# Kernel optimization log

Measured on AMD Instinct MI355X. Metric: run time of the kernel, lower is better.

## Reference

```python
import jax, jax.numpy as jnp
import numpy as np

B, IN_DIM, MEM = 8192, 4096, 256
MIN_TS, MAX_TS, EPS = 0.1, 10.0, 1e-6
LN_EPS = 1e-5


def setup_inputs() -> dict:
    key = jax.random.key(0)
    ks = jax.random.split(key, 10)
    std = 0.02
    d_in = MEM + IN_DIM  # 4352
    return {
        "x": jax.random.normal(ks[0], (B, IN_DIM), jnp.float32),
        "h": jax.random.normal(ks[1], (B, MEM), jnp.float32),
        # memory_target: Linear(d_in, 2*MEM) -> LN -> GELU -> Linear(2*MEM, MEM)
        "W1": std * jax.random.normal(ks[2], (d_in, 2 * MEM), jnp.float32),
        "b1": jnp.zeros((2 * MEM,), jnp.float32),
        "g1": jnp.ones((2 * MEM,), jnp.float32),
        "be1": jnp.zeros((2 * MEM,), jnp.float32),
        "W2": std * jax.random.normal(ks[3], (2 * MEM, MEM), jnp.float32),
        "b2": jnp.zeros((MEM,), jnp.float32),
        # decay_gate: Linear(d_in, MEM) -> sigmoid
        "Wd": std * jax.random.normal(ks[4], (d_in, MEM), jnp.float32),
        "bd": jnp.zeros((MEM,), jnp.float32),
        # input_gate: Linear(d_in, MEM) -> sigmoid
        "Wu": std * jax.random.normal(ks[5], (d_in, MEM), jnp.float32),
        "bu": jnp.zeros((MEM,), jnp.float32),
    }


def _layernorm(t, g, b):
    mu = jnp.mean(t, axis=-1, keepdims=True)
    var = jnp.mean(jnp.square(t - mu), axis=-1, keepdims=True)
    return (t - mu) * jax.lax.rsqrt(var + LN_EPS) * g + b


def reference(x, h, W1, b1, g1, be1, W2, b2, Wd, bd, Wu, bu):
    combined = jnp.concatenate([h, x], axis=-1)  # [B, MEM+IN_DIM]
    # memory_target branch: Linear -> LayerNorm -> GELU (exact) -> Linear -> tanh
    t = _layernorm(combined @ W1 + b1, g1, be1)
    t = jax.nn.gelu(t, approximate=False)
    h_candidate = jnp.tanh(t @ W2 + b2)  # [B, MEM]
    # gates
    decay = jax.nn.sigmoid(combined @ Wd + bd)
    update = jax.nn.sigmoid(combined @ Wu + bu)
    decay = MIN_TS + (MAX_TS - MIN_TS) * decay + EPS
    new_h = (1.0 - update) * (h / decay) + update * h_candidate
    # normalize_memory: rescale new_h to old h's L2 norm
    h_norm = jnp.maximum(jnp.linalg.norm(h, axis=-1, keepdims=True), EPS)
    nh_norm = jnp.maximum(jnp.linalg.norm(new_h, axis=-1, keepdims=True), 1e-12)
    new_h = new_h / nh_norm * h_norm
    return new_h
```

## Files before the change

### kernel.cpp

```cpp
#include <hip/hip_runtime.h>
#include <stdint.h>

typedef unsigned short u16;

#define B_ROWS 8192
#define IN_DIM 4096
#define MEM 256
#define D_IN 4352
#define N1 1024
#define K2 512
#define LN_EPS 1e-5f

typedef __attribute__((ext_vector_type(4))) float f32x4;
typedef __attribute__((ext_vector_type(4))) uint32_t u32x4;
typedef __attribute__((ext_vector_type(4))) unsigned short u16x4;
typedef __attribute__((ext_vector_type(8))) short bf16x8;

#define AS1(p) ((__attribute__((address_space(1))) void*)(p))
#define AS3(p) ((__attribute__((address_space(3))) void*)(p))

__device__ __forceinline__ float bf2f(u16 u) {
  union { uint32_t u; float f; } c; c.u = ((uint32_t)u) << 16; return c.f;
}
__device__ __forceinline__ u16 f2bf(float f) {
  union { float f; uint32_t u; } c; c.f = f;
  uint32_t r = (c.u + 0x7fffu + ((c.u >> 16) & 1u)) >> 16;
  return (u16)r;
}
__device__ __forceinline__ uint32_t fbits(float f) {
  union { float f; uint32_t u; } c; c.f = f; return c.u;
}
__device__ __forceinline__ uint32_t pack_rne(float a, float b) {
  return ((uint32_t)f2bf(b) << 16) | f2bf(a);
}
__device__ __forceinline__ uint32_t pack_trunc(float a, float b) {
  return (fbits(b) & 0xFFFF0000u) | (fbits(a) >> 16);
}

__global__ __launch_bounds__(256)
void prep_kernel(const float* __restrict__ W1, const float* __restrict__ Wd,
                 const float* __restrict__ Wu, const float* __restrict__ W2,
                 const float* __restrict__ h, const float* __restrict__ x,
                 u16* __restrict__ WT, u16* __restrict__ W2F, u16* __restrict__ Abf) {
  __shared__ u16 tile[64][68];
  const int blk = blockIdx.x, t = threadIdx.x;
  if (blk < 1088) {
    int n0 = (blk & 15) * 64, k0 = (blk >> 4) * 64;
    const float* src; int srcN, ns0;
    if (n0 < 512)      { src = W1; srcN = 512; ns0 = n0; }
    else if (n0 < 768) { src = Wd; srcN = 256; ns0 = n0 - 512; }
    else               { src = Wu; srcN = 256; ns0 = n0 - 768; }
    int rr = t >> 4;
    int c4 = (t & 15) * 4;
#pragma unroll
    for (int i = 0; i < 4; i++) {
      int k = i * 16 + rr;
      f32x4 v = *(const f32x4*)&src[(size_t)(k0 + k) * srcN + ns0 + c4];
      tile[c4 + 0][k] = f2bf(v[0]);
      tile[c4 + 1][k] = f2bf(v[1]);
      tile[c4 + 2][k] = f2bf(v[2]);
      tile[c4 + 3][k] = f2bf(v[3]);
    }
    __syncthreads();
#pragma unroll
    for (int i = 0; i < 4; i++) {
      int n = i * 16 + rr;
      u16x4 w;
      w.x = tile[n][c4 + 0];
      w.y = tile[n][c4 + 1];
      w.z = tile[n][c4 + 2];
      w.w = tile[n][c4 + 3];
      *(u16x4*)&WT[(size_t)(n0 + n) * D_IN + k0 + c4] = w;
    }
  } else if (blk < 1104) {
    int kw = blk - 1088;
#pragma unroll
    for (int q = 0; q < 4; q++) {
      float v[8];
#pragma unroll
      for (int j = 0; j < 8; j++)
        v[j] = W2[(size_t)(kw * 32 + q * 8 + j) * 256 + t];
      u32x4 w;
      w.x = pack_rne(v[0], v[1]);
      w.y = pack_rne(v[2], v[3]);
      w.z = pack_rne(v[4], v[5]);
      w.w = pack_rne(v[6], v[7]);
      *(u32x4*)&W2F[(size_t)((kw * 4 + q) * 256 + t) * 8] = w;
    }
  } else {
    int b = blk - 1104;
    const float* src; int r, dcol;
    if (b < 1024) {
      int g = (b * 256 + t) * 8;
      src = h + g; r = g >> 8; dcol = g & 255;
    } else {
      int g = ((b - 1024) * 256 + t) * 8;
      src = x + g; r = g >> 12; dcol = MEM + (g & 4095);
    }
    f32x4 v0 = *(const f32x4*)src;
    f32x4 v1 = *(const f32x4*)(src + 4);
    u32x4 w;
    w.x = pack_rne(v0[0], v0[1]);
    w.y = pack_rne(v0[2], v0[3]);
    w.z = pack_rne(v1[0], v1[1]);
    w.w = pack_rne(v1[2], v1[3]);
    *(u32x4*)&Abf[(size_t)r * D_IN + dcol] = w;
  }
}

__global__ __launch_bounds__(256, 4)
void gemm1_pre_kernel(const u16* __restrict__ Abf, const u16* __restrict__ WT,
                      u16* __restrict__ G0, u16* __restrict__ G1, int klen) {
  __shared__ __attribute__((aligned(16))) u16 As[128 * 64];
  __shared__ __attribute__((aligned(16))) u16 Bs[128 * 64];
  const int t = threadIdx.x;
  const int lane = t & 63, wave = t >> 6;
  const int by = blockIdx.x & 63;
  const int bx = (blockIdx.x >> 6) & 7;
  const int part = blockIdx.x >> 9;
  const int kbase = part * klen;
  u16* __restrict__ Gout = part ? G1 : G0;
  const int row0 = by * 128, col0 = bx * 128;
  const int q = lane >> 4, mrow = lane & 15;
  const int wm = wave >> 1, wn = wave & 1;

  int ar[4], ac[4];
#pragma unroll
  for (int j = 0; j < 4; j++) {
    int idx = j * 256 + t;
    int r = idx >> 3;
    ar[j] = r;
    ac[j] = (idx & 7) ^ (r & 7);
  }

  f32x4 acc[4][4] = {};

  for (int k0 = kbase; k0 < kbase + klen; k0 += 64) {
#pragma unroll
    for (int j = 0; j < 4; j++) {
      const u16* gp = WT + (size_t)(col0 + ar[j]) * D_IN + k0 + ac[j] * 8;
      __builtin_amdgcn_global_load_lds(AS1(gp), AS3(&Bs[(j * 256 + t) * 8]), 16, 0, 0);
    }
#pragma unroll
    for (int j = 0; j < 4; j++) {
      const u16* gp = Abf + (size_t)(row0 + ar[j]) * D_IN + k0 + ac[j] * 8;
      __builtin_amdgcn_global_load_lds(AS1(gp), AS3(&As[(j * 256 + t) * 8]), 16, 0, 0);
    }
    __syncthreads();
#pragma unroll
    for (int kk = 0; kk < 2; kk++) {
      bf16x8 a[4], b[4];
#pragma unroll
      for (int mt = 0; mt < 4; mt++) {
        int row = wm * 64 + mt * 16 + mrow;
        int p = (kk * 4 + q) ^ (mrow & 7);
        a[mt] = *(const bf16x8*)&As[row * 64 + p * 8];
      }
#pragma unroll
      for (int nt = 0; nt < 4; nt++) {
        int row = wn * 64 + nt * 16 + mrow;
        int p = (kk * 4 + q) ^ (mrow & 7);
        b[nt] = *(const bf16x8*)&Bs[row * 64 + p * 8];
      }
#pragma unroll
      for (int mt = 0; mt < 4; mt++) {
#pragma unroll
        for (int nt = 0; nt < 4; nt++) {
          acc[mt][nt] = __builtin_amdgcn_mfma_f32_16x16x32_bf16(a[mt], b[nt], acc[mt][nt], 0, 0, 0);
        }
      }
    }
    __syncthreads();
  }
#pragma unroll
  for (int mt = 0; mt < 4; mt++) {
#pragma unroll
    for (int nt = 0; nt < 4; nt++) {
#pragma unroll
      for (int i = 0; i < 4; i++) {
        int row = row0 + wm * 64 + mt * 16 + q * 4 + i;
        int col = col0 + wn * 64 + nt * 16 + mrow;
        Gout[(size_t)row * N1 + col] = f2bf(acc[mt][nt][i]);
      }
    }
  }
}

__global__ __launch_bounds__(256, 4)
void gemm1_inline_kernel(const float* __restrict__ x, const float* __restrict__ h,
                         const u16* __restrict__ WT, u16* __restrict__ G0,
                         u16* __restrict__ G1, int klen) {
  __shared__ __attribute__((aligned(16))) u16 As[128 * 64];
  __shared__ __attribute__((aligned(16))) u16 Bs[128 * 64];
  const int t = threadIdx.x;
  const int lane = t & 63, wave = t >> 6;
  const int by = blockIdx.x & 63;
  const int bx = (blockIdx.x >> 6) & 7;
  const int part = blockIdx.x >> 9;
  const int kbase = part * klen;
  u16* __restrict__ Gout = part ? G1 : G0;
  const int row0 = by * 128, col0 = bx * 128;
  const int q = lane >> 4, mrow = lane & 15;
  const int wm = wave >> 1, wn = wave & 1;

  int ar[4], ac[4];
#pragma unroll
  for (int j = 0; j < 4; j++) {
    int idx = j * 256 + t;
    int r = idx >> 3;
    ar[j] = r;
    ac[j] = (idx & 7) ^ (r & 7);
  }
  f32x4 acc[4][4] = {};
  for (int k0 = kbase; k0 < kbase + klen; k0 += 64) {
#pragma unroll
    for (int j = 0; j < 4; j++) {
      const u16* gp = WT + (size_t)(col0 + ar[j]) * D_IN + k0 + ac[j] * 8;
      __builtin_amdgcn_global_load_lds(AS1(gp), AS3(&Bs[(j * 256 + t) * 8]), 16, 0, 0);
    }
#pragma unroll
    for (int j = 0; j < 4; j++) {
      int k = k0 + ac[j] * 8;
      const float* gp = (k < MEM) ? (h + (size_t)(row0 + ar[j]) * MEM + k)
                                  : (x + (size_t)(row0 + ar[j]) * IN_DIM + (k - MEM));
      f32x4 v0 = *(const f32x4*)gp;
      f32x4 v1 = *(const f32x4*)(gp + 4);
      u32x4 w;
      w.x = pack_trunc(v0[0], v0[1]);
      w.y = pack_trunc(v0[2], v0[3]);
      w.z = pack_trunc(v1[0], v1[1]);
      w.w = pack_trunc(v1[2], v1[3]);
      *(u32x4*)&As[(j * 256 + t) * 8] = w;
    }
    __syncthreads();
#pragma unroll
    for (int kk = 0; kk < 2; kk++) {
      bf16x8 a[4], b[4];
#pragma unroll
      for (int mt = 0; mt < 4; mt++) {
        int row = wm * 64 + mt * 16 + mrow;
        int p = (kk * 4 + q) ^ (mrow & 7);
        a[mt] = *(const bf16x8*)&As[row * 64 + p * 8];
      }
#pragma unroll
      for (int nt = 0; nt < 4; nt++) {
        int row = wn * 64 + nt * 16 + mrow;
        int p = (kk * 4 + q) ^ (mrow & 7);
        b[nt] = *(const bf16x8*)&Bs[row * 64 + p * 8];
      }
#pragma unroll
      for (int mt = 0; mt < 4; mt++) {
#pragma unroll
        for (int nt = 0; nt < 4; nt++) {
          acc[mt][nt] = __builtin_amdgcn_mfma_f32_16x16x32_bf16(a[mt], b[nt], acc[mt][nt], 0, 0, 0);
        }
      }
    }
    __syncthreads();
  }
#pragma unroll
  for (int mt = 0; mt < 4; mt++) {
#pragma unroll
    for (int nt = 0; nt < 4; nt++) {
#pragma unroll
      for (int i = 0; i < 4; i++) {
        int row = row0 + wm * 64 + mt * 16 + q * 4 + i;
        int col = col0 + wn * 64 + nt * 16 + mrow;
        Gout[(size_t)row * N1 + col] = f2bf(acc[mt][nt][i]);
      }
    }
  }
}

__global__ __launch_bounds__(256, 4)
void fused_ln_gemm2_kernel(const u16* __restrict__ G0, const u16* __restrict__ G1,
                           const u16* __restrict__ W2F, const float* __restrict__ h,
                           const float* __restrict__ b1v, const float* __restrict__ g1v,
                           const float* __restrict__ be1v, const float* __restrict__ b2,
                           const float* __restrict__ bd, const float* __restrict__ bu,
                           float* __restrict__ out, int nparts) {
  __shared__ __attribute__((aligned(16))) u16 As[16 * 512];
  __shared__ float redA[16][4], redB[16][4], scl[16];
  const int t = threadIdx.x, lane = t & 63, wave = t >> 6;
  const int q = lane >> 4, mrow = lane & 15;
  const int r0 = blockIdx.x * 16;

  {
    const int lr = t & 15;
    const int lc = t >> 4;
    float z[32];
    const u16* g0p = G0 + (size_t)(r0 + lr) * N1 + lc * 32;
    const u16* g1p = G1 + (size_t)(r0 + lr) * N1 + lc * 32;
    float s = 0.f, ss = 0.f;
#pragma unroll
    for (int j = 0; j < 4; j++) {
      u32x4 w0 = *(const u32x4*)(g0p + j * 8);
      u32x4 w1;
      if (nparts == 2) w1 = *(const u32x4*)(g1p + j * 8);
#pragma unroll
      for (int e = 0; e < 4; e++) {
        float lo = bf2f((u16)(w0[e] & 0xffff));
        float hi = bf2f((u16)(w0[e] >> 16));
        if (nparts == 2) {
          lo += bf2f((u16)(w1[e] & 0xffff));
          hi += bf2f((u16)(w1[e] >> 16));
        }
        int cb = lc * 32 + j * 8 + e * 2;
        lo += b1v[cb];
        hi += b1v[cb + 1];
        z[j * 8 + e * 2] = lo;
        z[j * 8 + e * 2 + 1] = hi;
        s += lo + hi;
        ss += lo * lo + hi * hi;
      }
    }
    s += __shfl_xor(s, 16, 64);  s += __shfl_xor(s, 32, 64);
    ss += __shfl_xor(ss, 16, 64); ss += __shfl_xor(ss, 32, 64);
    if (lane < 16) { redA[lr][wave] = s; redB[lr][wave] = ss; }
    __syncthreads();
    float S  = redA[lr][0] + redA[lr][1] + redA[lr][2] + redA[lr][3];
    float SS = redB[lr][0] + redB[lr][1] + redB[lr][2] + redB[lr][3];
    float mu = S * (1.0f / 512.0f);
    float var = SS * (1.0f / 512.0f) - mu * mu;
    float rstd = rsqrtf(var + LN_EPS);
#pragma unroll
    for (int j = 0; j < 4; j++) {
      u32x4 wpk;
#pragma unroll
      for (int e = 0; e < 4; e++) {
        int cb = lc * 32 + j * 8 + e * 2;
        float y0 = (z[j * 8 + e * 2] - mu) * rstd * g1v[cb] + be1v[cb];
        float y1 = (z[j * 8 + e * 2 + 1] - mu) * rstd * g1v[cb + 1] + be1v[cb + 1];
        float o0 = 0.5f * y0 * (1.0f + erff(y0 * 0.7071067811865475f));
        float o1 = 0.5f * y1 * (1.0f + erff(y1 * 0.7071067811865475f));
        wpk[e] = pack_rne(o0, o1);
      }
      int p = lc * 4 + j;
      int ps = p ^ (lr & 7);
      *(u32x4*)&As[lr * 512 + ps * 8] = wpk;
    }
  }
  __syncthreads();

  f32x4 acc[4] = {};
#pragma unroll
  for (int kw = 0; kw < 16; kw++) {
    int pa = (kw * 4 + q) ^ (mrow & 7);
    bf16x8 a = *(const bf16x8*)&As[mrow * 512 + pa * 8];
#pragma unroll
    for (int nt = 0; nt < 4; nt++) {
      const u16* bp = W2F + (size_t)((kw * 4 + q) * 256 + wave * 64 + nt * 16 + mrow) * 8;
      bf16x8 b = *(const bf16x8*)bp;
      acc[nt] = __builtin_amdgcn_mfma_f32_16x16x32_bf16(a, b, acc[nt], 0, 0, 0);
    }
  }
  __syncthreads();

  float snh[4], shh[4];
#pragma unroll
  for (int i = 0; i < 4; i++) {
    int r = q * 4 + i;
    size_t grow = (size_t)(r0 + r);
    float a_nh = 0.f, a_h = 0.f;
#pragma unroll
    for (int nt = 0; nt < 4; nt++) {
      int c = wave * 64 + nt * 16 + mrow;
      float hc = tanhf(acc[nt][i] + b2[c]);
      float zd = bf2f(G0[grow * N1 + 512 + c]);
      float zu = bf2f(G0[grow * N1 + 768 + c]);
      if (nparts == 2) {
        zd += bf2f(G1[grow * N1 + 512 + c]);
        zu += bf2f(G1[grow * N1 + 768 + c]);
      }
      zd += bd[c];
      zu += bu[c];
      float dec = 0.1f + 9.9f / (1.0f + expf(-zd)) + 1e-6f;
      float u = 1.0f / (1.0f + expf(-zu));
      float hv = h[grow * MEM + c];
      float nh = (1.0f - u) * (hv / dec) + u * hc;
      acc[nt][i] = nh;
      a_nh += nh * nh;
      a_h += hv * hv;
    }
    snh[i] = a_nh;
    shh[i] = a_h;
  }
#pragma unroll
  for (int m = 1; m <= 8; m <<= 1) {
#pragma unroll
    for (int i = 0; i < 4; i++) {
      snh[i] += __shfl_xor(snh[i], m, 64);
      shh[i] += __shfl_xor(shh[i], m, 64);
    }
  }
  if (mrow == 0) {
#pragma unroll
    for (int i = 0; i < 4; i++) {
      int r = q * 4 + i;
      redA[r][wave] = snh[i];
      redB[r][wave] = shh[i];
    }
  }
  __syncthreads();
  if (t < 16) {
    float tn = redA[t][0] + redA[t][1] + redA[t][2] + redA[t][3];
    float th = redB[t][0] + redB[t][1] + redB[t][2] + redB[t][3];
    float hn = fmaxf(sqrtf(th), 1e-6f);
    float nn = fmaxf(sqrtf(tn), 1e-12f);
    scl[t] = hn / nn;
  }
  __syncthreads();
#pragma unroll
  for (int i = 0; i < 4; i++) {
    int r = q * 4 + i;
    size_t grow = (size_t)(r0 + r);
    float sc = scl[r];
#pragma unroll
    for (int nt = 0; nt < 4; nt++) {
      int c = wave * 64 + nt * 16 + mrow;
      out[grow * MEM + c] = acc[nt][i] * sc;
    }
  }
}

extern "C" void kernel_launch(void* const* d_in, const int* in_sizes, int n_in,
                              void* d_out, int out_size, void* d_ws, size_t ws_size,
                              hipStream_t stream) {
  const float* x   = (const float*)d_in[0];
  const float* h   = (const float*)d_in[1];
  const float* W1  = (const float*)d_in[2];
  const float* b1  = (const float*)d_in[3];
  const float* g1  = (const float*)d_in[4];
  const float* be1 = (const float*)d_in[5];
  const float* W2  = (const float*)d_in[6];
  const float* b2  = (const float*)d_in[7];
  const float* Wd  = (const float*)d_in[8];
  const float* bd  = (const float*)d_in[9];
  const float* Wu  = (const float*)d_in[10];
  const float* bu  = (const float*)d_in[11];
  float* out = (float*)d_out;

  char* ws = (char*)d_ws;
  u16* WT  = (u16*)(ws);
  u16* W2F = (u16*)(ws + 8912896);
  u16* G0  = (u16*)(ws + 9175040);
  u16* G1  = (u16*)(ws + 25952256);
  u16* Abf = (u16*)(ws + 42729472);

  const int nparts = (ws_size >= 42729472u) ? 2 : 1;
  const int klen = D_IN / nparts;
  const bool use_pre = (ws_size >= 114032640u);

  if (use_pre) {
    prep_kernel<<<18512, 256, 0, stream>>>(W1, Wd, Wu, W2, h, x, WT, W2F, Abf);
    gemm1_pre_kernel<<<512 * nparts, 256, 0, stream>>>(Abf, WT, G0, G1, klen);
  } else {
    prep_kernel<<<1104, 256, 0, stream>>>(W1, Wd, Wu, W2, h, x, WT, W2F, Abf);
    gemm1_inline_kernel<<<512 * nparts, 256, 0, stream>>>(x, h, WT, G0, G1, klen);
  }

  fused_ln_gemm2_kernel<<<B_ROWS / 16, 256, 0, stream>>>(G0, G1, W2F, h, b1, g1, be1,
                                                         b2, bd, bu, out, nparts);
}
```

Measured before the change: 338.5 us.

## Replace GEMM1 with 256x256-tile double-buffered pipelined kernel with block swizzle

Replaces the 128x128 single-buffered first GEMM with a 512-thread kernel computing 256x256 tiles. It double-buffers LDS, interleaves async global-to-LDS loads with MFMA phases using explicit vmcnt waits and barriers, and raises wave priority during MFMA. A block-index swizzle groups blocks for cache locality. The aim is to hide load latency and raise arithmetic intensity. In exchange it uses 128KB of LDS per block, larger accumulator register use, and launches only 256 blocks, so occupancy and load balance are at risk.

```diff
diff --git a/kernel.cpp b/kernel.cpp
--- a/kernel.cpp
+++ b/kernel.cpp
@@ -108,83 +108,128 @@
   }
 }
 
-__global__ __launch_bounds__(256, 4)
-void gemm1_pre_kernel(const u16* __restrict__ Abf, const u16* __restrict__ WT,
-                      u16* __restrict__ G0, u16* __restrict__ G1, int klen) {
-  __shared__ __attribute__((aligned(16))) u16 As[128 * 64];
-  __shared__ __attribute__((aligned(16))) u16 Bs[128 * 64];
+#define BAR() { asm volatile("" ::: "memory"); __builtin_amdgcn_s_barrier(); asm volatile("" ::: "memory"); }
+#define VMW4() asm volatile("s_waitcnt vmcnt(4)" ::: "memory");
+#define VMW0() asm volatile("s_waitcnt vmcnt(0)" ::: "memory");
+
+__global__ __launch_bounds__(512, 2)
+void gemm1_pre256_kernel(const u16* __restrict__ Abf, const u16* __restrict__ WT,
+                         u16* __restrict__ G0, u16* __restrict__ G1, int klen) {
+  __shared__ __attribute__((aligned(16))) u16 As[2][16384];
+  __shared__ __attribute__((aligned(16))) u16 Bs[2][16384];
   const int t = threadIdx.x;
   const int lane = t & 63, wave = t >> 6;
-  const int by = blockIdx.x & 63;
-  const int bx = (blockIdx.x >> 6) & 7;
-  const int part = blockIdx.x >> 9;
+  const int bid = (int)blockIdx.x;
+  const int swz = (bid & 7) * 32 + (bid >> 3);
+  const int by = swz & 31;
+  const int bx = (swz >> 5) & 3;
+  const int part = swz >> 7;
   const int kbase = part * klen;
   u16* __restrict__ Gout = part ? G1 : G0;
-  const int row0 = by * 128, col0 = bx * 128;
+  const int row0 = by * 256, col0 = bx * 256;
   const int q = lane >> 4, mrow = lane & 15;
-  const int wm = wave >> 1, wn = wave & 1;
-
-  int ar[4], ac[4];
-#pragma unroll
-  for (int j = 0; j < 4; j++) {
-    int idx = j * 256 + t;
-    int r = idx >> 3;
-    ar[j] = r;
-    ac[j] = (idx & 7) ^ (r & 7);
-  }
-
-  f32x4 acc[4][4] = {};
-
-  for (int k0 = kbase; k0 < kbase + klen; k0 += 64) {
-#pragma unroll
-    for (int j = 0; j < 4; j++) {
-      const u16* gp = WT + (size_t)(col0 + ar[j]) * D_IN + k0 + ac[j] * 8;
-      __builtin_amdgcn_global_load_lds(AS1(gp), AS3(&Bs[(j * 256 + t) * 8]), 16, 0, 0);
-    }
-#pragma unroll
-    for (int j = 0; j < 4; j++) {
-      const u16* gp = Abf + (size_t)(row0 + ar[j]) * D_IN + k0 + ac[j] * 8;
-      __builtin_amdgcn_global_load_lds(AS1(gp), AS3(&As[(j * 256 + t) * 8]), 16, 0, 0);
-    }
-    __syncthreads();
-#pragma unroll
-    for (int kk = 0; kk < 2; kk++) {
-      bf16x8 a[4], b[4];
-#pragma unroll
-      for (int mt = 0; mt < 4; mt++) {
-        int row = wm * 64 + mt * 16 + mrow;
-        int p = (kk * 4 + q) ^ (mrow & 7);
-        a[mt] = *(const bf16x8*)&As[row * 64 + p * 8];
-      }
-#pragma unroll
-      for (int nt = 0; nt < 4; nt++) {
-        int row = wn * 64 + nt * 16 + mrow;
-        int p = (kk * 4 + q) ^ (mrow & 7);
-        b[nt] = *(const bf16x8*)&Bs[row * 64 + p * 8];
-      }
-#pragma unroll
-      for (int mt = 0; mt < 4; mt++) {
-#pragma unroll
-        for (int nt = 0; nt < 4; nt++) {
-          acc[mt][nt] = __builtin_amdgcn_mfma_f32_16x16x32_bf16(a[mt], b[nt], acc[mt][nt], 0, 0, 0);
-        }
-      }
-    }
-    __syncthreads();
-  }
-#pragma unroll
-  for (int mt = 0; mt < 4; mt++) {
+  const int wm = wave >> 2, wn = wave & 3;
+  const int NT = klen >> 6;
+
+  int sr0, sc0_, sr1, sc1_;
+  {
+    int idx0 = t;        sr0 = idx0 >> 2; sc0_ = (idx0 & 3) ^ ((sr0 >> 1) & 3);
+    int idx1 = 512 + t;  sr1 = idx1 >> 2; sc1_ = (idx1 & 3) ^ ((sr1 >> 1) & 3);
+  }
+  const u16* pa0 = Abf + (size_t)(row0 + sr0) * D_IN + sc0_ * 8;
+  const u16* pa1 = Abf + (size_t)(row0 + sr1) * D_IN + sc1_ * 8;
+  const u16* pb0 = WT  + (size_t)(col0 + sr0) * D_IN + sc0_ * 8;
+  const u16* pb1 = WT  + (size_t)(col0 + sr1) * D_IN + sc1_ * 8;
+  const int fsw = (mrow >> 1) & 3;
+
+#define STAGE_A(buf, kk, kt)                                                            \
+  __builtin_amdgcn_global_load_lds(AS1(pa0 + (kt) + (kk) * 32),                         \
+      AS3(&As[buf][(kk) * 8192 + t * 8]), 16, 0, 0);                                    \
+  __builtin_amdgcn_global_load_lds(AS1(pa1 + (kt) + (kk) * 32),                         \
+      AS3(&As[buf][(kk) * 8192 + (512 + t) * 8]), 16, 0, 0);
+#define STAGE_B(buf, kk, kt)                                                            \
+  __builtin_amdgcn_global_load_lds(AS1(pb0 + (kt) + (kk) * 32),                         \
+      AS3(&Bs[buf][(kk) * 8192 + t * 8]), 16, 0, 0);                                    \
+  __builtin_amdgcn_global_load_lds(AS1(pb1 + (kt) + (kk) * 32),                         \
+      AS3(&Bs[buf][(kk) * 8192 + (512 + t) * 8]), 16, 0, 0);
+
+  f32x4 acc[8][4] = {};
+
+  STAGE_A(0, 0, kbase)
+  STAGE_B(0, 0, kbase)
+  STAGE_A(0, 1, kbase)
+  STAGE_B(0, 1, kbase)
+  VMW4();
+  BAR();
+
+  for (int tt = 0; tt < NT; ++tt) {
+    const int cur = tt & 1, nxt = cur ^ 1;
+    const int kn = kbase + (tt + 1) * 64;
+    const bool pf = (tt + 1 < NT);
+    bf16x8 a[4], b[4];
+
+#define READ_B(kk)                                                                      \
+  _Pragma("unroll") for (int nt = 0; nt < 4; nt++) {                                    \
+    int crow = wn * 64 + nt * 16 + mrow;                                                \
+    b[nt] = *(const bf16x8*)&Bs[cur][(kk) * 8192 + crow * 32 + (q ^ fsw) * 8];          \
+  }
+#define READ_A(kk, mh)                                                                  \
+  _Pragma("unroll") for (int i = 0; i < 4; i++) {                                       \
+    int arow = wm * 128 + ((mh) * 4 + i) * 16 + mrow;                                   \
+    a[i] = *(const bf16x8*)&As[cur][(kk) * 8192 + arow * 32 + (q ^ fsw) * 8];           \
+  }
+#define MFMA16(mh)                                                                      \
+  __builtin_amdgcn_s_setprio(1);                                                        \
+  _Pragma("unroll") for (int i = 0; i < 4; i++)                                         \
+    _Pragma("unroll") for (int nt = 0; nt < 4; nt++)                                    \
+      acc[(mh) * 4 + i][nt] =                                                           \
+          __builtin_amdgcn_mfma_f32_16x16x32_bf16(a[i], b[nt], acc[(mh) * 4 + i][nt], 0, 0, 0); \
+  __builtin_amdgcn_s_setprio(0);
+
+    READ_B(0)
+    READ_A(0, 0)
+    if (pf) { STAGE_A(nxt, 0, kn) }
+    BAR();
+    MFMA16(0)
+    BAR();
+    READ_A(0, 1)
+    if (pf) { STAGE_B(nxt, 0, kn) }
+    BAR();
+    MFMA16(1)
+    if (pf) { VMW4(); } else { VMW0(); }
+    BAR();
+    READ_B(1)
+    READ_A(1, 0)
+    if (pf) { STAGE_A(nxt, 1, kn) }
+    BAR();
+    MFMA16(0)
+    BAR();
+    READ_A(1, 1)
+    if (pf) { STAGE_B(nxt, 1, kn) }
+    BAR();
+    MFMA16(1)
+    if (pf) { VMW4(); }
+    BAR();
+#undef READ_B
+#undef READ_A
+#undef MFMA16
+  }
+
+#pragma unroll
+  for (int mt = 0; mt < 8; mt++) {
 #pragma unroll
     for (int nt = 0; nt < 4; nt++) {
 #pragma unroll
       for (int i = 0; i < 4; i++) {
-        int row = row0 + wm * 64 + mt * 16 + q * 4 + i;
+        int row = row0 + wm * 128 + mt * 16 + q * 4 + i;
         int col = col0 + wn * 64 + nt * 16 + mrow;
         Gout[(size_t)row * N1 + col] = f2bf(acc[mt][nt][i]);
       }
     }
   }
 }
+#undef STAGE_A
+#undef STAGE_B
 
 __global__ __launch_bounds__(256, 4)
 void gemm1_inline_kernel(const float* __restrict__ x, const float* __restrict__ h,
@@ -449,11 +494,11 @@
 
   const int nparts = (ws_size >= 42729472u) ? 2 : 1;
   const int klen = D_IN / nparts;
-  const bool use_pre = (ws_size >= 114032640u);
+  const bool use_pre = (ws_size >= 114032640u) && (nparts == 2);
 
   if (use_pre) {
     prep_kernel<<<18512, 256, 0, stream>>>(W1, Wd, Wu, W2, h, x, WT, W2F, Abf);
-    gemm1_pre_kernel<<<512 * nparts, 256, 0, stream>>>(Abf, WT, G0, G1, klen);
+    gemm1_pre256_kernel<<<256, 512, 0, stream>>>(Abf, WT, G0, G1, klen);
   } else {
     prep_kernel<<<1104, 256, 0, stream>>>(W1, Wd, Wu, W2, h, x, WT, W2F, Abf);
     gemm1_inline_kernel<<<512 * nparts, 256, 0, stream>>>(x, h, WT, G0, G1, klen);
```

New measurement: 344.7 us. Within noise of the previous version (+1.8%).
